# Kernel optimization log

Hardware: AMD Instinct MI355X
Metric: run time of the kernel (lower is better)

Reference implementation:

```python
import jax, jax.numpy as jnp
import numpy as np

NUM_CLASSES = 10
SOFT_CENTER_RADIUS = 3.0
TOPK = 13
IOU_WEIGHT = 3.0
EPS = 1e-07
INF = 100000000.0


def setup_inputs() -> dict:
    key = jax.random.key(0)
    ks = jax.random.split(key, 8)
    B, N, G, C = 8, 16384, 64, NUM_CLASSES
    # priors: [N,4] = (cx, cy, stride_x, stride_y)
    centers = jax.random.uniform(ks[0], (N, 2), minval=0.0, maxval=640.0)
    strides = jnp.full((N, 2), 16.0, dtype=jnp.float32)
    priors = jnp.concatenate([centers, strides], axis=-1)
    # 2D gt boxes (x1,y1,x2,y2) inside a 640px image
    xy = jax.random.uniform(ks[1], (B, G, 2), minval=0.0, maxval=520.0)
    wh = jax.random.uniform(ks[2], (B, G, 2), minval=20.0, maxval=120.0)
    gt_bboxes = jnp.concatenate([xy, xy + wh], axis=-1)
    gt_center = xy + 0.5 * wh
    # 3D boxes: only columns [0,2] (x,z) are used by the dist iou branch
    gt_bboxes_3d = jax.random.normal(ks[3], (B, G, 7)) * 2.0
    pred_bboxes = jax.random.normal(ks[4], (B, N, 7)) * 2.0
    pred_scores = jax.random.normal(ks[5], (B, N, C))
    gt_labels = jax.random.randint(ks[6], (B, G, 1), 0, C, dtype=jnp.int32)
    pad_bbox_flag = jnp.ones((B, G, 1), dtype=jnp.float32)
    return dict(pred_bboxes=pred_bboxes, pred_scores=pred_scores, priors=priors,
                gt_labels=gt_labels, gt_bboxes=gt_bboxes, gt_center=gt_center,
                gt_bboxes_3d=gt_bboxes_3d, pad_bbox_flag=pad_bbox_flag)


def reference(pred_bboxes, pred_scores, priors, gt_labels, gt_bboxes, gt_center,
              gt_bboxes_3d, pad_bbox_flag):
    B, N, _ = pred_bboxes.shape
    G = gt_bboxes.shape[1]

    pc = priors[:, :2]                                   # [N,2]
    # find_inside_points: prior center strictly inside 2D gt box -> [B,N,G]
    cx, cy = pc[None, :, None, 0], pc[None, :, None, 1]
    inside = ((cx > gt_bboxes[:, None, :, 0]) & (cy > gt_bboxes[:, None, :, 1]) &
              (cx < gt_bboxes[:, None, :, 2]) & (cy < gt_bboxes[:, None, :, 3]))
    is_in_gts = inside.astype(jnp.float32) * pad_bbox_flag[:, None, :, 0]  # [B,N,G]
    mask = is_in_gts > 0

    # soft center prior
    strides = priors[None, :, None, 2:]                  # [1,N,1,2]
    diff = (pc[None, :, None, :] - gt_center[:, None, :, :]) / strides
    distance = jnp.linalg.norm(diff, axis=-1) * is_in_gts
    soft_center_prior = 10.0 ** (distance - SOFT_CENTER_RADIUS)

    # dist-type pairwise iou on (x,z) plane
    xz = jnp.array([0, 2])
    pxz = pred_bboxes[:, :, xz]                          # [B,N,2]
    gxz = gt_bboxes_3d[:, :, xz]                         # [B,G,2]
    d = jnp.linalg.norm(pxz[:, :, None, :] - gxz[:, None, :, :], axis=-1)
    pairwise_ious = jnp.clip(1.0 - d / 4.0, 0.0, 1.0)    # [B,N,G]

    iou_cost = -jnp.log(pairwise_ious + EPS) * IOU_WEIGHT

    labels = gt_labels[..., 0]                           # [B,G]
    idx = jnp.broadcast_to(labels[:, None, :], (B, N, G))
    pscores = jnp.take_along_axis(pred_scores, idx, axis=2)  # [B,N,G] logits
    scale = pairwise_ious - jax.nn.sigmoid(pscores)
    # stable BCE-with-logits(pscores, target=pairwise_ious)
    bce = jnp.maximum(pscores, 0.0) - pscores * pairwise_ious + jnp.log1p(jnp.exp(-jnp.abs(pscores)))
    cls_cost = bce * scale ** 2

    cost = jnp.where(mask, cls_cost + iou_cost + soft_center_prior, INF)

    # ---- dynamic k matching ----
    k = min(TOPK, N)
    topk_ious = jax.lax.top_k(jnp.swapaxes(pairwise_ious, 1, 2), k)[0]  # [B,G,k]
    dynamic_ks = jnp.clip(topk_ious.sum(-1).astype(jnp.int32), 1, None)  # [B,G]
    sorted_cost = jnp.sort(cost, axis=1)
    cost_k = jnp.take_along_axis(sorted_cost, dynamic_ks[:, None, :], axis=1)
    cost_k_1 = jnp.take_along_axis(sorted_cost, (dynamic_ks - 1)[:, None, :], axis=1)
    thr = 0.5 * (cost_k + cost_k_1) * is_in_gts          # [B,N,G]
    matching = cost <= thr                               # bool [B,N,G]
    masked_cost = jnp.where(matching, cost, INF)
    multi = matching.sum(-1) > 1                         # prior matched to >1 gt
    argmin_gt = jnp.argmin(masked_cost, axis=2)
    onehot = jax.nn.one_hot(argmin_gt, G, dtype=jnp.bool_)
    matching = jnp.where(multi[..., None], onehot, matching)

    # ---- assemble outputs (dense, jit-friendly version of nonzero indices) ----
    max_index = jnp.argmin(cost, axis=2)                 # [B,N]
    assign_metrics = jnp.take_along_axis(pairwise_ious, max_index[..., None], axis=2)[..., 0]
    matched = matching.any(-1)                           # [B,N]
    gt_idx = jnp.argmax(matching, axis=-1)               # [B,N]
    matched_iou = jnp.take_along_axis(pairwise_ious, gt_idx[..., None], axis=2)[..., 0]
    assign_metrics = jnp.where(matched, matched_iou, assign_metrics)

    assigned_labels = jnp.take_along_axis(labels, max_index, axis=1)  # [B,N]
    assigned_labels = jnp.where(assign_metrics < 1e-07, NUM_CLASSES, assigned_labels)
    assigned_labels = jnp.where(matched, jnp.take_along_axis(labels, gt_idx, axis=1), assigned_labels)

    assigned_labels_weights = jnp.ones((B, N), dtype=jnp.float32)
    return assigned_labels, assigned_labels_weights, assign_metrics, matching
```

## Files before the change

### kernel.cpp

```cpp
#include <hip/hip_runtime.h>
#include <hip/hip_bf16.h>
#include <stdint.h>

#define NCLS 10
#define B_ 8
#define N_ 16384
#define G_ 64
#define INF_ 1.0e8f
#define CAP_ 768
#define CSTRIDE 16

typedef unsigned long long u64;
typedef unsigned int u32;

__device__ __forceinline__ u32 ordf(float f) {
    u32 b = __float_as_uint(f);
    return (b & 0x80000000u) ? ~b : (b | 0x80000000u);
}
__device__ __forceinline__ float unordf(u32 u) {
    u32 b = (u & 0x80000000u) ? (u ^ 0x80000000u) : ~u;
    return __uint_as_float(b);
}

__device__ __forceinline__ float iou_pair(float px, float pz, float g3x, float g3z) {
#pragma clang fp contract(off)
    float ddx = px - g3x;
    float ddz = pz - g3z;
    float d = sqrtf(ddx * ddx + ddz * ddz);
    float iou = 1.0f - d / 4.0f;
    return fminf(fmaxf(iou, 0.0f), 1.0f);
}

__device__ __forceinline__ float cost_pair(float cx, float cy, float sx, float sy,
                                           float ps, float gcx, float gcy,
                                           float pad, float iou) {
#pragma clang fp contract(off)
    float dx = (cx - gcx) / sx;
    float dy = (cy - gcy) / sy;
    float dist = sqrtf(dx * dx + dy * dy) * pad;
    float soft = exp10f(dist - 3.0f);
    float iou_cost = -logf(iou + 1e-7f) * 3.0f;
    float e = expf(-fabsf(ps));
    float sig = (ps >= 0.0f) ? (1.0f / (1.0f + e)) : (e / (1.0f + e));
    float scale = iou - sig;
    float bce = fmaxf(ps, 0.0f) - ps * iou + log1pf(e);
    float cls = bce * (scale * scale);
    return cls + iou_cost + soft;
}

__device__ __forceinline__ u32 wave_max_u32(u32 k) {
#pragma unroll
    for (int off = 32; off >= 1; off >>= 1) {
        u32 o = __shfl_xor(k, off, 64);
        k = (o > k) ? o : k;
    }
    return k;
}
__device__ __forceinline__ u32 wave_min_u32(u32 k) {
#pragma unroll
    for (int off = 32; off >= 1; off >>= 1) {
        u32 o = __shfl_xor(k, off, 64);
        k = (o < k) ? o : k;
    }
    return k;
}

__global__ __launch_bounds__(256) void k_ab(
    const float* __restrict__ priors,
    const float* __restrict__ gt_bboxes,
    const float* __restrict__ pad_flag,
    const float* __restrict__ pred_bboxes,
    const float* __restrict__ gt_b3d,
    u64* __restrict__ mask64,
    u32* __restrict__ cnt,
    u32* __restrict__ bucket,
    float* __restrict__ iou13)
{
    u32 r5 = blockIdx.x % 5u, q5 = blockIdx.x / 5u;
    if (r5 == 4u) {
        int b = q5 >> 6;
        int n = ((q5 & 63) << 8) | threadIdx.x;
        float4 pr = ((const float4*)priors)[n];
        float cx = pr.x, cy = pr.y;
        u64 m = 0;
#pragma unroll 8
        for (int g = 0; g < G_; ++g) {
            int gi = b * G_ + g;
            float4 gbb = ((const float4*)gt_bboxes)[gi];
            float padv = pad_flag[gi];
            bool isin = (cx > gbb.x) && (cy > gbb.y) && (cx < gbb.z) && (cy < gbb.w)
                        && (padv > 0.0f);
            m |= ((u64)isin) << g;
        }
        mask64[(size_t)b * N_ + n] = m;

        u64 mm = m;
        while (mm) {
            int g = __ffsll(mm) - 1;
            mm &= mm - 1;
            int gi = b * G_ + g;
            u32 p = atomicAdd(&cnt[gi * CSTRIDE], 1u);
            if (p < CAP_) bucket[(size_t)gi * CAP_ + p] = (u32)n;
        }
    } else {
        int c = (int)(q5 * 4u + r5);
        int wid = (c << 2) | (threadIdx.x >> 6);
        int lane = threadIdx.x & 63;
        int b = wid >> 10;
        int g = (wid >> 4) & 63;
        int chunk = wid & 15;
        int gi = b * G_ + g;
        float g3x = gt_b3d[gi * 7 + 0];
        float g3z = gt_b3d[gi * 7 + 2];
        const float* pb = pred_bboxes + (size_t)b * N_ * 7;

        float s[16];
        int n0 = chunk * 1024 + lane;
#pragma unroll
        for (int it = 0; it < 16; ++it) {
            int n = n0 + it * 64;
            s[it] = iou_pair(pb[n * 7 + 0], pb[n * 7 + 2], g3x, g3z);
        }
#pragma unroll
        for (int p = 1; p < 16; p <<= 1) {
#pragma unroll
            for (int k = p; k >= 1; k >>= 1) {
#pragma unroll
                for (int j = k % p; j <= 15 - k; j += 2 * k) {
#pragma unroll
                    for (int i = 0; i < k; ++i) {
                        if (i + j + k <= 15) {
                            if ((i + j) / (2 * p) == (i + j + k) / (2 * p)) {
                                float hi = fmaxf(s[i + j], s[i + j + k]);
                                float lo = fminf(s[i + j], s[i + j + k]);
                                s[i + j] = hi; s[i + j + k] = lo;
                            }
                        }
                    }
                }
            }
        }
        float keepv = 0.0f;
        for (int r = 0; r < 13; ++r) {
            u32 mykey = ordf(s[0]);
            u32 m = wave_max_u32(mykey);
            if (lane == r) keepv = unordf(m);
            int winner = __ffsll(__ballot(mykey == m)) - 1;
            if (lane == winner) {
#pragma unroll
                for (int j = 0; j < 13; ++j) s[j] = s[j + 1];
            }
        }
        if (lane < 13) iou13[(size_t)gi * 208 + chunk * 13 + lane] = keepv;
    }
}

__global__ __launch_bounds__(64) void k1c(
    const float* __restrict__ iou13,
    const u32*   __restrict__ cnt,
    const u32*   __restrict__ bucket,
    const float* __restrict__ priors,
    const float* __restrict__ pred_bboxes,
    const float* __restrict__ pred_scores,
    const int*   __restrict__ gt_labels,
    const float* __restrict__ gt_center,
    const float* __restrict__ gt_b3d,
    const float* __restrict__ pad_flag,
    float* __restrict__ thr_half)
{
    int gi = blockIdx.x;
    int lane = threadIdx.x;
    int b = gi >> 6;

    const float* base = iou13 + (size_t)gi * 208;
    float v0 = base[lane];
    float v1 = base[64 + lane];
    float v2 = base[128 + lane];
    float v3 = (lane < 16) ? base[192 + lane] : -3.0e38f;
    { float h = fmaxf(v0, v1), l = fminf(v0, v1); v0 = h; v1 = l; }
    { float h = fmaxf(v2, v3), l = fminf(v2, v3); v2 = h; v3 = l; }
    { float h = fmaxf(v0, v2), l = fminf(v0, v2); v0 = h; v2 = l; }
    { float h = fmaxf(v1, v3), l = fminf(v1, v3); v1 = h; v3 = l; }
    { float h = fmaxf(v1, v2), l = fminf(v1, v2); v1 = h; v2 = l; }
    float sum13 = 0.0f;
    for (int r = 0; r < 13; ++r) {
        u32 mykey = ordf(v0);
        u32 m = wave_max_u32(mykey);
        sum13 += unordf(m);
        int winner = __ffsll(__ballot(mykey == m)) - 1;
        if (lane == winner) { v0 = v1; v1 = v2; v2 = v3; v3 = -3.0e38f; }
    }
    int ks = (int)sum13;
    if (ks < 1) ks = 1;

    float gcx = gt_center[gi * 2 + 0], gcy = gt_center[gi * 2 + 1];
    float g3x = gt_b3d[gi * 7 + 0],   g3z = gt_b3d[gi * 7 + 2];
    float padv = pad_flag[gi];
    int lab = gt_labels[gi];
    const float* pb = pred_bboxes + (size_t)b * N_ * 7;
    const float* sc = pred_scores + (size_t)b * N_ * 10;

    u32 c = cnt[gi * CSTRIDE];
    if (c > CAP_) c = CAP_;
    float l[14];
#pragma unroll
    for (int j = 0; j < 14; ++j) l[j] = INF_;
    for (u32 idx = lane; idx < c; idx += 64) {
        int n = (int)bucket[(size_t)gi * CAP_ + idx];
        float4 pr = ((const float4*)priors)[n];
        float px = pb[n * 7 + 0];
        float pz = pb[n * 7 + 2];
        float ps = sc[n * 10 + lab];
        float iou = iou_pair(px, pz, g3x, g3z);
        float cst = cost_pair(pr.x, pr.y, pr.z, pr.w, ps, gcx, gcy, padv, iou);
        if (cst < l[13]) {
            float v = cst;
#pragma unroll
            for (int j = 0; j < 14; ++j) {
                float o = l[j]; bool lt = v < o;
                float mn = lt ? v : o; v = lt ? o : v; l[j] = mn;
            }
        }
    }
    float ck = INF_, ckm1 = INF_;
    for (int r = 0; r < 14; ++r) {
        u32 mykey = ordf(l[0]);
        u32 m = wave_min_u32(mykey);
        float vm = unordf(m);
        if (r == ks - 1) ckm1 = vm;
        if (r == ks)     ck = vm;
        int winner = __ffsll(__ballot(mykey == m)) - 1;
        if (lane == winner) {
#pragma unroll
            for (int j = 0; j < 13; ++j) l[j] = l[j + 1];
            l[13] = INF_;
        }
    }
    if (lane == 0) thr_half[gi] = 0.5f * (ck + ckm1);
}

__global__ __launch_bounds__(256) void k2(
    const float* __restrict__ priors,
    const float* __restrict__ pred_bboxes,
    const float* __restrict__ pred_scores,
    const int*   __restrict__ gt_labels,
    const float* __restrict__ gt_center,
    const float* __restrict__ gt_b3d,
    const float* __restrict__ pad_flag,
    const float* __restrict__ thr_half,
    const u64*   __restrict__ mask64,
    float* __restrict__ out)
{
    __shared__ float s_gcx[G_], s_gcy[G_], s_g3x[G_], s_g3z[G_];
    __shared__ float s_pad[G_], s_thr[G_];
    __shared__ int   s_lab[G_];
    __shared__ u64   s_words[256];

    int b = blockIdx.x >> 6;
    int n0b = (blockIdx.x & 63) << 8;
    int n = n0b | threadIdx.x;
    size_t t = (size_t)b * N_ + n;

    if (threadIdx.x < G_) {
        int gi = b * G_ + threadIdx.x;
        s_gcx[threadIdx.x] = gt_center[gi * 2 + 0];
        s_gcy[threadIdx.x] = gt_center[gi * 2 + 1];
        s_g3x[threadIdx.x] = gt_b3d[gi * 7 + 0];
        s_g3z[threadIdx.x] = gt_b3d[gi * 7 + 2];
        s_pad[threadIdx.x] = pad_flag[gi];
        s_thr[threadIdx.x] = thr_half[gi];
        s_lab[threadIdx.x] = gt_labels[gi];
    }
    __syncthreads();

    const float* pb = pred_bboxes + (size_t)b * N_ * 7;
    const float* sc = pred_scores + (size_t)b * N_ * 10;
    float4 pr = ((const float4*)priors)[n];
    float px = pb[n * 7 + 0];
    float pz = pb[n * 7 + 2];

    float iouC = iou_pair(px, pz, s_g3x[0], s_g3z[0]);
    float costC = INF_;
    int   labC = s_lab[0];

    float iouM = 0.0f, costM = 3.0e38f;
    int   labM = 0, argM = 0;
    u64 mmatch = 0;

    u64 m = mask64[t];
    while (m) {
        int g = __ffsll(m) - 1;
        m &= m - 1;
        float gcx = s_gcx[g], gcy = s_gcy[g];
        float g3x = s_g3x[g], g3z = s_g3z[g];
        float padg = s_pad[g];
        int   labg = s_lab[g];
        float th = s_thr[g];
        float ps = sc[n * 10 + labg];
        float iou = iou_pair(px, pz, g3x, g3z);
        float c = cost_pair(pr.x, pr.y, pr.z, pr.w, ps, gcx, gcy, padg, iou);
        if (c < costC) { costC = c; iouC = iou; labC = labg; }
        if (c <= th * padg) {
            mmatch |= 1ull << g;
            if (c < costM) { costM = c; iouM = iou; labM = labg; argM = g; }
        }
    }
    int cm = __popcll(mmatch);
    bool matched = cm > 0;
    u64 outm = (cm > 1) ? (1ull << argM) : mmatch;
    float metric = matched ? iouM : iouC;
    float olab = matched ? (float)labM
                         : ((iouC < 1e-7f) ? (float)NCLS : (float)labC);

    float* out_lab = out;
    float* out_w   = out + (size_t)B_ * N_;
    float* out_met = out + (size_t)2 * B_ * N_;
    float* out_mat = out + (size_t)3 * B_ * N_;
    out_lab[t] = olab;
    out_w[t]   = 1.0f;
    out_met[t] = metric;
    s_words[threadIdx.x] = outm;
    __syncthreads();

    int q  = threadIdx.x & 3;
    int r0 = threadIdx.x >> 2;
    size_t rowbase = (size_t)b * N_ + n0b;
#pragma unroll
    for (int it = 0; it < 4; ++it) {
        int row = r0 + (it << 6);
        u64 w = s_words[row];
        u32 bits = (u32)(w >> (q * 16)) & 0xffffu;
        float* dst = out_mat + (rowbase + row) * 64 + q * 16;
#pragma unroll
        for (int jj = 0; jj < 4; ++jj) {
            float4 f;
            f.x = (bits >> (jj * 4 + 0)) & 1u ? 1.0f : 0.0f;
            f.y = (bits >> (jj * 4 + 1)) & 1u ? 1.0f : 0.0f;
            f.z = (bits >> (jj * 4 + 2)) & 1u ? 1.0f : 0.0f;
            f.w = (bits >> (jj * 4 + 3)) & 1u ? 1.0f : 0.0f;
            ((float4*)dst)[jj] = f;
        }
    }
}

extern "C" void kernel_launch(void* const* d_in, const int* in_sizes, int n_in,
                              void* d_out, int out_size, void* d_ws, size_t ws_size,
                              hipStream_t stream)
{
    const float* pred_bboxes = (const float*)d_in[0];
    const float* pred_scores = (const float*)d_in[1];
    const float* priors      = (const float*)d_in[2];
    const int*   gt_labels   = (const int*)d_in[3];
    const float* gt_bboxes   = (const float*)d_in[4];
    const float* gt_center   = (const float*)d_in[5];
    const float* gt_b3d      = (const float*)d_in[6];
    const float* pad_flag    = (const float*)d_in[7];
    float* out = (float*)d_out;

    char* ws = (char*)d_ws;
    u32* cnt     = (u32*)ws;
    u32* bucket  = (u32*)(ws + 32768);
    u64* mask64  = (u64*)(ws + 32768 + 1572864);
    float* iou13 = (float*)(ws + 32768 + 1572864 + 1048576);
    float* thr_half = (float*)(ws + 32768 + 1572864 + 1048576 + 425984);

    hipMemsetAsync(cnt, 0, 512 * CSTRIDE * sizeof(u32), stream);
    k_ab<<<2560, 256, 0, stream>>>(priors, gt_bboxes, pad_flag, pred_bboxes,
                                   gt_b3d, mask64, cnt, bucket, iou13);
    k1c<<<512, 64, 0, stream>>>(iou13, cnt, bucket, priors, pred_bboxes,
                                pred_scores, gt_labels, gt_center, gt_b3d,
                                pad_flag, thr_half);
    k2<<<512, 256, 0, stream>>>(priors, pred_bboxes, pred_scores, gt_labels,
                                gt_center, gt_b3d, pad_flag,
                                thr_half, mask64, out);
}
```

Measured before the change: 79.64 us.

## Fuse top-k IoU and cost threshold into one per-gt block kernel

Merges the IoU top-13 kernel and the cost-threshold kernel into one 256-thread block per gt. Each block scans all priors of its batch, keeps running top-13 IoU and top-14 in-box cost lists per thread, then reduces them across waves through shared memory. This drops the atomic bucket build, the memset, the intermediate iou13 buffer and one launch. In exchange every gt block rescans all 16384 priors, with serial insertion-sort inserts and extra priors reads, instead of reading only its bucketed in-box points.

```diff
diff --git a/kernel.cpp b/kernel.cpp
--- a/kernel.cpp
+++ b/kernel.cpp
@@ -7,8 +7,6 @@
 #define N_ 16384
 #define G_ 64
 #define INF_ 1.0e8f
-#define CAP_ 768
-#define CSTRIDE 16
 
 typedef unsigned long long u64;
 typedef unsigned int u32;
@@ -65,21 +63,25 @@
     return k;
 }
 
-__global__ __launch_bounds__(256) void k_ab(
+__global__ __launch_bounds__(256) void k1f(
     const float* __restrict__ priors,
     const float* __restrict__ gt_bboxes,
     const float* __restrict__ pad_flag,
     const float* __restrict__ pred_bboxes,
+    const float* __restrict__ pred_scores,
+    const int*   __restrict__ gt_labels,
+    const float* __restrict__ gt_center,
     const float* __restrict__ gt_b3d,
     u64* __restrict__ mask64,
-    u32* __restrict__ cnt,
-    u32* __restrict__ bucket,
-    float* __restrict__ iou13)
+    float* __restrict__ thr_half)
 {
-    u32 r5 = blockIdx.x % 5u, q5 = blockIdx.x / 5u;
-    if (r5 == 4u) {
-        int b = q5 >> 6;
-        int n = ((q5 & 63) << 8) | threadIdx.x;
+    int role = blockIdx.x & 1;
+    int idx  = blockIdx.x >> 1;
+    int tid  = threadIdx.x;
+
+    if (role == 1) {
+        int b = idx >> 6;
+        int n = ((idx & 63) << 8) | tid;
         float4 pr = ((const float4*)priors)[n];
         float cx = pr.x, cy = pr.y;
         u64 m = 0;
@@ -93,106 +95,18 @@
             m |= ((u64)isin) << g;
         }
         mask64[(size_t)b * N_ + n] = m;
-
-        u64 mm = m;
-        while (mm) {
-            int g = __ffsll(mm) - 1;
-            mm &= mm - 1;
-            int gi = b * G_ + g;
-            u32 p = atomicAdd(&cnt[gi * CSTRIDE], 1u);
-            if (p < CAP_) bucket[(size_t)gi * CAP_ + p] = (u32)n;
-        }
-    } else {
-        int c = (int)(q5 * 4u + r5);
-        int wid = (c << 2) | (threadIdx.x >> 6);
-        int lane = threadIdx.x & 63;
-        int b = wid >> 10;
-        int g = (wid >> 4) & 63;
-        int chunk = wid & 15;
-        int gi = b * G_ + g;
-        float g3x = gt_b3d[gi * 7 + 0];
-        float g3z = gt_b3d[gi * 7 + 2];
-        const float* pb = pred_bboxes + (size_t)b * N_ * 7;
-
-        float s[16];
-        int n0 = chunk * 1024 + lane;
-#pragma unroll
-        for (int it = 0; it < 16; ++it) {
-            int n = n0 + it * 64;
-            s[it] = iou_pair(pb[n * 7 + 0], pb[n * 7 + 2], g3x, g3z);
-        }
-#pragma unroll
-        for (int p = 1; p < 16; p <<= 1) {
-#pragma unroll
-            for (int k = p; k >= 1; k >>= 1) {
-#pragma unroll
-                for (int j = k % p; j <= 15 - k; j += 2 * k) {
-#pragma unroll
-                    for (int i = 0; i < k; ++i) {
-                        if (i + j + k <= 15) {
-                            if ((i + j) / (2 * p) == (i + j + k) / (2 * p)) {
-                                float hi = fmaxf(s[i + j], s[i + j + k]);
-                                float lo = fminf(s[i + j], s[i + j + k]);
-                                s[i + j] = hi; s[i + j + k] = lo;
-                            }
-                        }
-                    }
-                }
-            }
-        }
-        float keepv = 0.0f;
-        for (int r = 0; r < 13; ++r) {
-            u32 mykey = ordf(s[0]);
-            u32 m = wave_max_u32(mykey);
-            if (lane == r) keepv = unordf(m);
-            int winner = __ffsll(__ballot(mykey == m)) - 1;
-            if (lane == winner) {
-#pragma unroll
-                for (int j = 0; j < 13; ++j) s[j] = s[j + 1];
-            }
-        }
-        if (lane < 13) iou13[(size_t)gi * 208 + chunk * 13 + lane] = keepv;
-    }
-}
-
-__global__ __launch_bounds__(64) void k1c(
-    const float* __restrict__ iou13,
-    const u32*   __restrict__ cnt,
-    const u32*   __restrict__ bucket,
-    const float* __restrict__ priors,
-    const float* __restrict__ pred_bboxes,
-    const float* __restrict__ pred_scores,
-    const int*   __restrict__ gt_labels,
-    const float* __restrict__ gt_center,
-    const float* __restrict__ gt_b3d,
-    const float* __restrict__ pad_flag,
-    float* __restrict__ thr_half)
-{
-    int gi = blockIdx.x;
-    int lane = threadIdx.x;
+        return;
+    }
+
+    __shared__ float s_iou[4 * 13];
+    __shared__ float s_cost[4 * 14];
+    int gi = idx;
     int b = gi >> 6;
-
-    const float* base = iou13 + (size_t)gi * 208;
-    float v0 = base[lane];
-    float v1 = base[64 + lane];
-    float v2 = base[128 + lane];
-    float v3 = (lane < 16) ? base[192 + lane] : -3.0e38f;
-    { float h = fmaxf(v0, v1), l = fminf(v0, v1); v0 = h; v1 = l; }
-    { float h = fmaxf(v2, v3), l = fminf(v2, v3); v2 = h; v3 = l; }
-    { float h = fmaxf(v0, v2), l = fminf(v0, v2); v0 = h; v2 = l; }
-    { float h = fmaxf(v1, v3), l = fminf(v1, v3); v1 = h; v3 = l; }
-    { float h = fmaxf(v1, v2), l = fminf(v1, v2); v1 = h; v2 = l; }
-    float sum13 = 0.0f;
-    for (int r = 0; r < 13; ++r) {
-        u32 mykey = ordf(v0);
-        u32 m = wave_max_u32(mykey);
-        sum13 += unordf(m);
-        int winner = __ffsll(__ballot(mykey == m)) - 1;
-        if (lane == winner) { v0 = v1; v1 = v2; v2 = v3; v3 = -3.0e38f; }
-    }
-    int ks = (int)sum13;
-    if (ks < 1) ks = 1;
-
+    int lane = tid & 63;
+    int w = tid >> 6;
+
+    float gx1 = gt_bboxes[gi * 4 + 0], gy1 = gt_bboxes[gi * 4 + 1];
+    float gx2 = gt_bboxes[gi * 4 + 2], gy2 = gt_bboxes[gi * 4 + 3];
     float gcx = gt_center[gi * 2 + 0], gcy = gt_center[gi * 2 + 1];
     float g3x = gt_b3d[gi * 7 + 0],   g3z = gt_b3d[gi * 7 + 2];
     float padv = pad_flag[gi];
@@ -200,43 +114,100 @@
     const float* pb = pred_bboxes + (size_t)b * N_ * 7;
     const float* sc = pred_scores + (size_t)b * N_ * 10;
 
-    u32 c = cnt[gi * CSTRIDE];
-    if (c > CAP_) c = CAP_;
-    float l[14];
-#pragma unroll
-    for (int j = 0; j < 14; ++j) l[j] = INF_;
-    for (u32 idx = lane; idx < c; idx += 64) {
-        int n = (int)bucket[(size_t)gi * CAP_ + idx];
+    float ti[13], tc[14];
+#pragma unroll
+    for (int j = 0; j < 13; ++j) ti[j] = -1.0f;
+#pragma unroll
+    for (int j = 0; j < 14; ++j) tc[j] = INF_;
+
+    for (int it = 0; it < 64; ++it) {
+        int n = (it << 8) | tid;
         float4 pr = ((const float4*)priors)[n];
         float px = pb[n * 7 + 0];
         float pz = pb[n * 7 + 2];
-        float ps = sc[n * 10 + lab];
         float iou = iou_pair(px, pz, g3x, g3z);
-        float cst = cost_pair(pr.x, pr.y, pr.z, pr.w, ps, gcx, gcy, padv, iou);
-        if (cst < l[13]) {
-            float v = cst;
-#pragma unroll
-            for (int j = 0; j < 14; ++j) {
-                float o = l[j]; bool lt = v < o;
-                float mn = lt ? v : o; v = lt ? o : v; l[j] = mn;
+        if (iou > ti[12]) {
+            float v = iou;
+#pragma unroll
+            for (int j = 0; j < 13; ++j) {
+                float o = ti[j]; bool gt_ = v > o;
+                float mx = gt_ ? v : o; v = gt_ ? o : v; ti[j] = mx;
             }
         }
-    }
-    float ck = INF_, ckm1 = INF_;
-    for (int r = 0; r < 14; ++r) {
-        u32 mykey = ordf(l[0]);
-        u32 m = wave_min_u32(mykey);
-        float vm = unordf(m);
-        if (r == ks - 1) ckm1 = vm;
-        if (r == ks)     ck = vm;
-        int winner = __ffsll(__ballot(mykey == m)) - 1;
-        if (lane == winner) {
-#pragma unroll
-            for (int j = 0; j < 13; ++j) l[j] = l[j + 1];
-            l[13] = INF_;
-        }
-    }
-    if (lane == 0) thr_half[gi] = 0.5f * (ck + ckm1);
+        bool isin = (pr.x > gx1) && (pr.y > gy1) && (pr.x < gx2) && (pr.y < gy2)
+                    && (padv > 0.0f);
+        if (isin) {
+            float ps = sc[n * 10 + lab];
+            float cst = cost_pair(pr.x, pr.y, pr.z, pr.w, ps, gcx, gcy, padv, iou);
+            if (cst < tc[13]) {
+                float v = cst;
+#pragma unroll
+                for (int j = 0; j < 14; ++j) {
+                    float o = tc[j]; bool lt = v < o;
+                    float mn = lt ? v : o; v = lt ? o : v; tc[j] = mn;
+                }
+            }
+        }
+    }
+
+    {
+        float keepv = 0.0f;
+        for (int r = 0; r < 13; ++r) {
+            u32 mykey = ordf(ti[0]);
+            u32 m = wave_max_u32(mykey);
+            if (lane == r) keepv = unordf(m);
+            int winner = __ffsll(__ballot(mykey == m)) - 1;
+            if (lane == winner) {
+#pragma unroll
+                for (int j = 0; j < 12; ++j) ti[j] = ti[j + 1];
+                ti[12] = -3.0e38f;
+            }
+        }
+        if (lane < 13) s_iou[w * 13 + lane] = keepv;
+    }
+    {
+        float keepv = 0.0f;
+        for (int r = 0; r < 14; ++r) {
+            u32 mykey = ordf(tc[0]);
+            u32 m = wave_min_u32(mykey);
+            if (lane == r) keepv = unordf(m);
+            int winner = __ffsll(__ballot(mykey == m)) - 1;
+            if (lane == winner) {
+#pragma unroll
+                for (int j = 0; j < 13; ++j) tc[j] = tc[j + 1];
+                tc[13] = 3.0e38f;
+            }
+        }
+        if (lane < 14) s_cost[w * 14 + lane] = keepv;
+    }
+    __syncthreads();
+
+    if (w == 0) {
+        float vi = (lane < 52) ? s_iou[lane] : -3.0e38f;
+        float sum13 = 0.0f;
+        for (int r = 0; r < 13; ++r) {
+            u32 mykey = ordf(vi);
+            u32 m = wave_max_u32(mykey);
+            sum13 += unordf(m);
+            int winner = __ffsll(__ballot(mykey == m)) - 1;
+            if (lane == winner) vi = -3.0e38f;
+        }
+        int ks = (int)sum13;
+        if (ks < 1) ks = 1;
+
+        float vc = (lane < 56) ? s_cost[lane] : 3.0e38f;
+        float ck = INF_, ckm1 = INF_;
+        for (int r = 0; r < 14; ++r) {
+            u32 mykey = ordf(vc);
+            u32 m = wave_min_u32(mykey);
+            float vm = unordf(m);
+            if (r == ks - 1) ckm1 = vm;
+            if (r == ks)     ck = vm;
+            int winner = __ffsll(__ballot(mykey == m)) - 1;
+            if (lane == winner) vc = 3.0e38f;
+        }
+        if (lane == 0) thr_half[gi] = 0.5f * (ck + ckm1);
+    }
 }
 
 __global__ __launch_bounds__(256) void k2(
@@ -328,8 +299,8 @@
 #pragma unroll
     for (int it = 0; it < 4; ++it) {
         int row = r0 + (it << 6);
-        u64 w = s_words[row];
-        u32 bits = (u32)(w >> (q * 16)) & 0xffffu;
+        u64 wv = s_words[row];
+        u32 bits = (u32)(wv >> (q * 16)) & 0xffffu;
         float* dst = out_mat + (rowbase + row) * 64 + q * 16;
 #pragma unroll
         for (int jj = 0; jj < 4; ++jj) {
@@ -358,18 +329,12 @@
     float* out = (float*)d_out;
 
     char* ws = (char*)d_ws;
-    u32* cnt     = (u32*)ws;
-    u32* bucket  = (u32*)(ws + 32768);
-    u64* mask64  = (u64*)(ws + 32768 + 1572864);
-    float* iou13 = (float*)(ws + 32768 + 1572864 + 1048576);
-    float* thr_half = (float*)(ws + 32768 + 1572864 + 1048576 + 425984);
-
-    hipMemsetAsync(cnt, 0, 512 * CSTRIDE * sizeof(u32), stream);
-    k_ab<<<2560, 256, 0, stream>>>(priors, gt_bboxes, pad_flag, pred_bboxes,
-                                   gt_b3d, mask64, cnt, bucket, iou13);
-    k1c<<<512, 64, 0, stream>>>(iou13, cnt, bucket, priors, pred_bboxes,
-                                pred_scores, gt_labels, gt_center, gt_b3d,
-                                pad_flag, thr_half);
+    u64* mask64     = (u64*)ws;
+    float* thr_half = (float*)(ws + 1048576);
+
+    k1f<<<1024, 256, 0, stream>>>(priors, gt_bboxes, pad_flag, pred_bboxes,
+                                  pred_scores, gt_labels, gt_center, gt_b3d,
+                                  mask64, thr_half);
     k2<<<512, 256, 0, stream>>>(priors, pred_bboxes, pred_scores, gt_labels,
                                 gt_center, gt_b3d, pad_flag,
                                 thr_half, mask64, out);
```

Measured after the change: 164.7 us. 107% more time.

## Replace atomic per-GT candidate buckets with transposed ballot bitmaps

Applied to the files above, without the earlier changes.

The mask kernel now writes a per-GT transposed bitmap of inside priors via wave ballots, replacing the atomicAdd-based bucket lists. The memset of counters goes away. The top-k cost kernel scans 256 bitmap words per GT, with each lane walking its set bits. This removes atomic contention and the capacity cap, at the cost of 64 extra bitmap stores per wave and uneven per-lane work in k1c.

```diff
diff --git a/kernel.cpp b/kernel.cpp
--- a/kernel.cpp
+++ b/kernel.cpp
@@ -7,8 +7,6 @@
 #define N_ 16384
 #define G_ 64
 #define INF_ 1.0e8f
-#define CAP_ 768
-#define CSTRIDE 16
 
 typedef unsigned long long u64;
 typedef unsigned int u32;
@@ -72,18 +70,19 @@
     const float* __restrict__ pred_bboxes,
     const float* __restrict__ gt_b3d,
     u64* __restrict__ mask64,
-    u32* __restrict__ cnt,
-    u32* __restrict__ bucket,
+    u64* __restrict__ bitmapT,
     float* __restrict__ iou13)
 {
     u32 r5 = blockIdx.x % 5u, q5 = blockIdx.x / 5u;
+    int tid = threadIdx.x;
+    int lane = tid & 63;
     if (r5 == 4u) {
         int b = q5 >> 6;
-        int n = ((q5 & 63) << 8) | threadIdx.x;
+        int n = ((q5 & 63) << 8) | tid;
+        u32 wword = ((q5 & 63) << 2) | (u32)(tid >> 6);
         float4 pr = ((const float4*)priors)[n];
         float cx = pr.x, cy = pr.y;
         u64 m = 0;
-#pragma unroll 8
         for (int g = 0; g < G_; ++g) {
             int gi = b * G_ + g;
             float4 gbb = ((const float4*)gt_bboxes)[gi];
@@ -91,21 +90,13 @@
             bool isin = (cx > gbb.x) && (cy > gbb.y) && (cx < gbb.z) && (cy < gbb.w)
                         && (padv > 0.0f);
             m |= ((u64)isin) << g;
+            u64 bal = __ballot(isin);
+            if (lane == 0) bitmapT[(((size_t)gi) << 8) | wword] = bal;
         }
         mask64[(size_t)b * N_ + n] = m;
-
-        u64 mm = m;
-        while (mm) {
-            int g = __ffsll(mm) - 1;
-            mm &= mm - 1;
-            int gi = b * G_ + g;
-            u32 p = atomicAdd(&cnt[gi * CSTRIDE], 1u);
-            if (p < CAP_) bucket[(size_t)gi * CAP_ + p] = (u32)n;
-        }
     } else {
         int c = (int)(q5 * 4u + r5);
-        int wid = (c << 2) | (threadIdx.x >> 6);
-        int lane = threadIdx.x & 63;
+        int wid = (c << 2) | (tid >> 6);
         int b = wid >> 10;
         int g = (wid >> 4) & 63;
         int chunk = wid & 15;
@@ -157,8 +148,7 @@
 
 __global__ __launch_bounds__(64) void k1c(
     const float* __restrict__ iou13,
-    const u32*   __restrict__ cnt,
-    const u32*   __restrict__ bucket,
+    const u64*   __restrict__ bitmapT,
     const float* __restrict__ priors,
     const float* __restrict__ pred_bboxes,
     const float* __restrict__ pred_scores,
@@ -200,25 +190,31 @@
     const float* pb = pred_bboxes + (size_t)b * N_ * 7;
     const float* sc = pred_scores + (size_t)b * N_ * 10;
 
-    u32 c = cnt[gi * CSTRIDE];
-    if (c > CAP_) c = CAP_;
     float l[14];
 #pragma unroll
     for (int j = 0; j < 14; ++j) l[j] = INF_;
-    for (u32 idx = lane; idx < c; idx += 64) {
-        int n = (int)bucket[(size_t)gi * CAP_ + idx];
-        float4 pr = ((const float4*)priors)[n];
-        float px = pb[n * 7 + 0];
-        float pz = pb[n * 7 + 2];
-        float ps = sc[n * 10 + lab];
-        float iou = iou_pair(px, pz, g3x, g3z);
-        float cst = cost_pair(pr.x, pr.y, pr.z, pr.w, ps, gcx, gcy, padv, iou);
-        if (cst < l[13]) {
-            float v = cst;
-#pragma unroll
-            for (int j = 0; j < 14; ++j) {
-                float o = l[j]; bool lt = v < o;
-                float mn = lt ? v : o; v = lt ? o : v; l[j] = mn;
+#pragma unroll
+    for (int j = 0; j < 4; ++j) {
+        u32 w = (u32)(lane + 64 * j);
+        u64 wv = bitmapT[(((size_t)gi) << 8) | w];
+        u32 nb = w << 6;
+        while (wv) {
+            int bit = __ffsll(wv) - 1;
+            wv &= wv - 1;
+            int n = (int)(nb | (u32)bit);
+            float4 pr = ((const float4*)priors)[n];
+            float px = pb[n * 7 + 0];
+            float pz = pb[n * 7 + 2];
+            float ps = sc[n * 10 + lab];
+            float iou = iou_pair(px, pz, g3x, g3z);
+            float cst = cost_pair(pr.x, pr.y, pr.z, pr.w, ps, gcx, gcy, padv, iou);
+            if (cst < l[13]) {
+                float v = cst;
+#pragma unroll
+                for (int jj = 0; jj < 14; ++jj) {
+                    float o = l[jj]; bool lt = v < o;
+                    float mn = lt ? v : o; v = lt ? o : v; l[jj] = mn;
+                }
             }
         }
     }
@@ -328,8 +324,8 @@
 #pragma unroll
     for (int it = 0; it < 4; ++it) {
         int row = r0 + (it << 6);
-        u64 w = s_words[row];
-        u32 bits = (u32)(w >> (q * 16)) & 0xffffu;
+        u64 wv = s_words[row];
+        u32 bits = (u32)(wv >> (q * 16)) & 0xffffu;
         float* dst = out_mat + (rowbase + row) * 64 + q * 16;
 #pragma unroll
         for (int jj = 0; jj < 4; ++jj) {
@@ -358,16 +354,14 @@
     float* out = (float*)d_out;
 
     char* ws = (char*)d_ws;
-    u32* cnt     = (u32*)ws;
-    u32* bucket  = (u32*)(ws + 32768);
-    u64* mask64  = (u64*)(ws + 32768 + 1572864);
-    float* iou13 = (float*)(ws + 32768 + 1572864 + 1048576);
-    float* thr_half = (float*)(ws + 32768 + 1572864 + 1048576 + 425984);
-
-    hipMemsetAsync(cnt, 0, 512 * CSTRIDE * sizeof(u32), stream);
+    u64* mask64   = (u64*)ws;
+    u64* bitmapT  = (u64*)(ws + 1048576);
+    float* iou13  = (float*)(ws + 2097152);
+    float* thr_half = (float*)(ws + 2097152 + 425984);
+
     k_ab<<<2560, 256, 0, stream>>>(priors, gt_bboxes, pad_flag, pred_bboxes,
-                                   gt_b3d, mask64, cnt, bucket, iou13);
-    k1c<<<512, 64, 0, stream>>>(iou13, cnt, bucket, priors, pred_bboxes,
+                                   gt_b3d, mask64, bitmapT, iou13);
+    k1c<<<512, 64, 0, stream>>>(iou13, bitmapT, priors, pred_bboxes,
                                 pred_scores, gt_labels, gt_center, gt_b3d,
                                 pad_flag, thr_half);
     k2<<<512, 256, 0, stream>>>(priors, pred_bboxes, pred_scores, gt_labels,
```

Result: slower. 81.68 us (+2.6%).
